# Optimization experiments

Hardware: AMD Instinct MI355X
Metric: run time of the kernel (lower is better)

The kernel has to match this reference:

```python
import jax, jax.numpy as jnp
import numpy as np

NEG_SLOPE = 0.2

def gat_conv(x, edge_index, W, a_src, a_dst, b):
    # PyG GATConv, heads=1, eval mode (dropout off), add_self_loops=True
    N = x.shape[0]
    h = x @ W                                   # [N, C]
    loops = jnp.arange(N, dtype=edge_index.dtype)
    src = jnp.concatenate([edge_index[0], loops])
    dst = jnp.concatenate([edge_index[1], loops])
    s_src = h @ a_src                            # [N]
    s_dst = h @ a_dst                            # [N]
    e = s_src[src] + s_dst[dst]                  # [E+N]
    e = jnp.where(e > 0, e, NEG_SLOPE * e)       # leaky_relu
    # segment softmax over destination neighborhoods
    m = jax.ops.segment_max(e, dst, num_segments=N)
    ex = jnp.exp(e - m[dst])
    denom = jax.ops.segment_sum(ex, dst, num_segments=N)
    alpha = ex / denom[dst]                      # [E+N]
    out = jax.ops.segment_sum(alpha[:, None] * h[src], dst, num_segments=N)
    return out + b

def setup_inputs() -> dict:
    key = jax.random.key(0)
    ks = jax.random.split(key, 10)
    N, F_in, H, C, E = 100000, 256, 128, 40, 1600000
    x = jax.random.normal(ks[0], (N, F_in), dtype=jnp.float32)
    edge_index = jax.random.randint(ks[1], (2, E), 0, N, dtype=jnp.int64)
    s1 = 1.0 / np.sqrt(F_in)
    s2 = 1.0 / np.sqrt(H)
    W1 = jax.random.normal(ks[2], (F_in, H), dtype=jnp.float32) * s1
    a_src1 = jax.random.normal(ks[3], (H,), dtype=jnp.float32) * s2
    a_dst1 = jax.random.normal(ks[4], (H,), dtype=jnp.float32) * s2
    b1 = jnp.zeros((H,), dtype=jnp.float32)
    W2 = jax.random.normal(ks[5], (H, C), dtype=jnp.float32) * s2
    a_src2 = jax.random.normal(ks[6], (C,), dtype=jnp.float32) * 0.1
    a_dst2 = jax.random.normal(ks[7], (C,), dtype=jnp.float32) * 0.1
    b2 = jnp.zeros((C,), dtype=jnp.float32)
    return {"x": x, "edge_index": edge_index, "W1": W1, "a_src1": a_src1,
            "a_dst1": a_dst1, "b1": b1, "W2": W2, "a_src2": a_src2,
            "a_dst2": a_dst2, "b2": b2}

def reference(x, edge_index, W1, a_src1, a_dst1, b1, W2, a_src2, a_dst2, b2):
    h = gat_conv(x, edge_index, W1, a_src1, a_dst1, b1)
    h = jax.nn.relu(h)
    # dropout(p=0.6) is identity in eval mode
    h = gat_conv(h, edge_index, W2, a_src2, a_dst2, b2)
    return jax.nn.log_softmax(h, axis=1)
```

## Files before the change

kernel.cpp:

```cpp
#include <hip/hip_runtime.h>
#include <math.h>

#define NEG_SLOPE 0.2f
#define CAP 64
#define NB 64
#define NBUCKET 1563
#define BCAP 1408
#define CHUNK 8192
#define NBINBLK 196

typedef __attribute__((ext_vector_type(8))) short short8;
typedef __attribute__((ext_vector_type(4))) short short4v;
typedef __attribute__((ext_vector_type(4))) float f32x4;
typedef __attribute__((ext_vector_type(2))) float f32x2;

__device__ inline unsigned short f2bf(float f) {
    union { float f; unsigned u; } x; x.f = f;
    unsigned r = x.u + 0x7FFFu + ((x.u >> 16) & 1u);
    return (unsigned short)(r >> 16);
}

__device__ __forceinline__ void gload_lds16(const void* g, void* l) {
    __builtin_amdgcn_global_load_lds(
        (const __attribute__((address_space(1))) void*)g,
        (__attribute__((address_space(3))) void*)l, 16, 0, 0);
}


__global__ __launch_bounds__(256) void front_kernel(
    const int* __restrict__ ei, int* __restrict__ bcnt,
    unsigned* __restrict__ bbuf, int E,
    const float* __restrict__ W1, const float* __restrict__ W2,
    short* __restrict__ bsw1, short* __restrict__ bsw2)
{
    __shared__ int lc[NBUCKET];
    __shared__ int lsrc[CHUNK];
    __shared__ int ldst[CHUNK];
    const int tid = threadIdx.x;

    if (blockIdx.x < NBINBLK) {
        const int base = blockIdx.x * CHUNK;
        const int n = (E - base < CHUNK) ? (E - base) : CHUNK;

        for (int b = tid; b < NBUCKET; b += 256) lc[b] = 0;
        __syncthreads();

        for (int i = tid; i < n; i += 256) {
            int s = ei[base + i];
            int d = ei[E + base + i];
            lsrc[i] = s;
            ldst[i] = d;
            atomicAdd(&lc[d >> 6], 1);
        }
        __syncthreads();

        for (int b = tid; b < NBUCKET; b += 256) {
            int c = lc[b];
            lc[b] = c ? atomicAdd(&bcnt[b], c) : 0;
        }
        __syncthreads();

        for (int i = tid; i < n; i += 256) {
            int s = lsrc[i];
            int d = ldst[i];
            int b = d >> 6;
            int pos = atomicAdd(&lc[b], 1);
            if (pos < BCAP)
                bbuf[(size_t)b * BCAP + pos] = (unsigned)s | ((unsigned)(d & 63) << 17);
        }
    } else {
        int t = (blockIdx.x - NBINBLK) * 256 + tid;
        if (t < 4096) {
            int lane = t & 63;
            int f = t >> 6;
            int k_step = f & 7;
            int n_tile = f >> 3;
            int n  = n_tile * 16 + (lane & 15);
            int k0 = k_step * 32 + (lane >> 4) * 8;
            short8 v;
            #pragma unroll
            for (int j = 0; j < 8; j++)
                v[j] = (short)f2bf(W1[(size_t)(k0 + j) * 128 + n]);
            ((short8*)bsw1)[t] = v;
        } else if (t < 4096 + 768) {
            int u = t - 4096;
            int lane = u & 63;
            int f = u >> 6;
            int k_step = f & 3;
            int n_tile = f >> 2;
            int n  = n_tile * 16 + (lane & 15);
            int k0 = k_step * 32 + (lane >> 4) * 8;
            short8 v;
            #pragma unroll
            for (int j = 0; j < 8; j++)
                v[j] = (n < 40) ? (short)f2bf(W2[(size_t)(k0 + j) * 40 + n]) : (short)0;
            ((short8*)bsw2)[u] = v;
        }
    }
}

__global__ __launch_bounds__(256) void mid_kernel(
    const int* __restrict__ bcnt, const unsigned* __restrict__ bbuf,
    int* __restrict__ csr, int* __restrict__ sorted, int* __restrict__ clsCnt,
    const float* __restrict__ x, const short* __restrict__ bsw,
    const float* __restrict__ a_src, const float* __restrict__ a_dst,
    unsigned char* __restrict__ h1, float* __restrict__ s_src,
    float* __restrict__ s_dst, int M)
{
    __shared__ __align__(16) char smem[16896];
    const int tid = threadIdx.x;

    if (blockIdx.x < NBUCKET) {
        int* lcnt = (int*)smem;
        int (*lcsr)[CAP] = (int(*)[CAP])(smem + 256);
        int* chist = (int*)(smem + 256 + 16384);
        int* cbase = (int*)(smem + 256 + 16384 + 16);

        const int b = blockIdx.x;
        const int nb = b * NB;

        if (tid < NB) lcnt[tid] = 0;
        if (tid < 4) chist[tid] = 0;
        __syncthreads();

        if (tid < NB && nb + tid < M) {
            int pos = atomicAdd(&lcnt[tid], 1);
            if (pos < CAP) lcsr[tid][pos] = nb + tid;
        }

        int ne = bcnt[b]; if (ne > BCAP) ne = BCAP;
        const unsigned* __restrict__ bp = bbuf + (size_t)b * BCAP;
        for (int j = tid; j < ne; j += 256) {
            unsigned v = bp[j];
            int s  = v & 0x1FFFF;
            int dl = v >> 17;
            int pos = atomicAdd(&lcnt[dl], 1);
            if (pos < CAP) lcsr[dl][pos] = s;
        }
        __syncthreads();

        const int4* __restrict__ srcp = (const int4*)&lcsr[0][0];
        int4* __restrict__ dstp = (int4*)(csr + (size_t)nb * CAP);
        #pragma unroll 4
        for (int j = tid; j < NB * CAP / 4; j += 256) dstp[j] = srcp[j];

        int deg = 0, cls = 0, pos = 0;
        bool isNode = (tid < NB && nb + tid < M);
        if (isNode) {
            deg = lcnt[tid]; if (deg > CAP) deg = CAP;
            cls = (deg - 1) >> 4;
            pos = atomicAdd(&chist[cls], 1);
        }
        __syncthreads();
        if (tid < 4) cbase[tid] = chist[tid] ? atomicAdd(&clsCnt[tid], chist[tid]) : 0;
        __syncthreads();
        if (isNode)
            sorted[(size_t)cls * M + cbase[cls] + pos] = (nb + tid) | (deg << 17);
        return;
    }

    const int wave = tid >> 6, lane = tid & 63;
    short8* lbs = (short8*)smem;
    const int rowBase = (blockIdx.x - NBUCKET) * 64;
    const int arow = rowBase + wave * 16 + (lane & 15);
    const int acol0 = (lane >> 4) * 8;
    const bool rv = (arow < M);
    const float* __restrict__ xr = x + (size_t)arow * 256 + acol0;
    const char* __restrict__ bsb = (const char*)bsw;

    auto stage = [&](int buf, int nt) {
        const char* s = bsb + nt * 8192 + wave * 2048 + lane * 16;
        char* d = smem + buf * 8192 + wave * 2048 + lane * 16;
        gload_lds16(s, d);
        gload_lds16(s + 1024, d + 1024);
    };

    stage(0, 0);

    short8 a[8];
    #pragma unroll
    for (int k = 0; k < 8; k++) {
        float4 p = make_float4(0.f, 0.f, 0.f, 0.f);
        float4 q = p;
        if (rv) {
            p = *(const float4*)(xr + k * 32);
            q = *(const float4*)(xr + k * 32 + 4);
        }
        short8 t;
        t[0] = (short)f2bf(p.x); t[1] = (short)f2bf(p.y);
        t[2] = (short)f2bf(p.z); t[3] = (short)f2bf(p.w);
        t[4] = (short)f2bf(q.x); t[5] = (short)f2bf(q.y);
        t[6] = (short)f2bf(q.z); t[7] = (short)f2bf(q.w);
        a[k] = t;
    }

    const int R0 = rowBase + wave * 16 + (lane >> 4) * 4;
    const int Cb = lane & 15;

    float asv[8], adv[8];
    #pragma unroll
    for (int nt = 0; nt < 8; nt++) {
        asv[nt] = a_src[nt * 16 + Cb];
        adv[nt] = a_dst[nt * 16 + Cb];
    }

    stage(1, 1);

    float ss[4] = {0.f, 0.f, 0.f, 0.f};
    float sd[4] = {0.f, 0.f, 0.f, 0.f};
    f32x4 prev = {0.f, 0.f, 0.f, 0.f};
    int wpk[4][4];

    #pragma unroll
    for (int nt = 0; nt < 8; nt++) {
        if (nt == 7) asm volatile("s_waitcnt vmcnt(0)" ::: "memory");
        else         asm volatile("s_waitcnt vmcnt(2)" ::: "memory");
        __builtin_amdgcn_s_barrier();

        short8 breg[8];
        #pragma unroll
        for (int k = 0; k < 8; k++) breg[k] = lbs[(nt & 1) * 512 + k * 64 + lane];
        asm volatile("s_waitcnt lgkmcnt(0)" ::: "memory");
        __builtin_amdgcn_sched_barrier(0);
        __builtin_amdgcn_s_barrier();

        if (nt < 6) stage(nt & 1, nt + 2);

        f32x4 acc = {0.f, 0.f, 0.f, 0.f};
        #pragma unroll
        for (int k = 0; k < 8; k++)
            acc = __builtin_amdgcn_mfma_f32_16x16x32_bf16(a[k], breg[k], acc, 0, 0, 0);

        float as_ = asv[nt], ad_ = adv[nt];
        #pragma unroll
        for (int r = 0; r < 4; r++) {
            float v = acc[r];
            ss[r] = fmaf(v, as_, ss[r]);
            sd[r] = fmaf(v, ad_, sd[r]);
        }
        if (nt & 1) {
            #pragma unroll
            for (int r = 0; r < 4; r++)
                wpk[nt >> 1][r] = __builtin_amdgcn_cvt_pk_fp8_f32(prev[r], acc[r], 0, false);
        } else {
            prev = acc;
        }
    }

    #pragma unroll
    for (int r = 0; r < 4; r++) {
        int R = R0 + r;
        if (R < M) {
            #pragma unroll
            for (int t = 0; t < 4; t++)
                *(unsigned short*)(h1 + (size_t)R * 128 + t * 32 + 2 * Cb) =
                    (unsigned short)wpk[t][r];
        }
    }
    #pragma unroll
    for (int off = 1; off < 16; off <<= 1) {
        #pragma unroll
        for (int r = 0; r < 4; r++) {
            ss[r] += __shfl_xor(ss[r], off);
            sd[r] += __shfl_xor(sd[r], off);
        }
    }
    if ((lane & 15) == 0) {
        #pragma unroll
        for (int r = 0; r < 4; r++) {
            int R = R0 + r;
            if (R < M) { s_src[R] = ss[r]; s_dst[R] = sd[r]; }
        }
    }
}

__global__ __launch_bounds__(256) void agg1_kernel(
    const unsigned char* __restrict__ h, const int* __restrict__ csr,
    const int* __restrict__ sorted, const int* __restrict__ clsCnt,
    const float* __restrict__ s_src, const float* __restrict__ s_dst,
    const float* __restrict__ bias,
    const short* __restrict__ bsw2,
    const float* __restrict__ a_src2, const float* __restrict__ a_dst2,
    unsigned char* __restrict__ h2, float* __restrict__ ss2,
    float* __restrict__ sd2, int N)
{
    __shared__ short lrow[16][136];
    __shared__ int   lnode[16];
    const int tid = threadIdx.x;
    const int lane = tid & 63;
    const int c = lane & 15;
    const int base = lane & 48;
    const int grp = tid >> 4;
    const int g = blockIdx.x * 16 + grp;

    int c0 = clsCnt[0], c01 = c0 + clsCnt[1], c012 = c01 + clsCnt[2];
    int cls, local;
    if (g < c0)        { cls = 0; local = g; }
    else if (g < c01)  { cls = 1; local = g - c0; }
    else if (g < c012) { cls = 2; local = g - c01; }
    else               { cls = 3; local = g - c012; }

    int ent = sorted[(size_t)cls * N + local];
    int n = ent & 0x1FFFF;
    int deg = ent >> 17;
    const int* __restrict__ edges = csr + (size_t)n * CAP;
    float sdn = s_dst[n];

    int s0 = 0, s1 = 0, s2 = 0, s3 = 0;
    float e0 = -1e30f, e1 = -1e30f, e2 = -1e30f, e3 = -1e30f;
    if (c < deg)      { s0 = edges[c];      e0 = s_src[s0] + sdn; }
    if (c + 16 < deg) { s1 = edges[c + 16]; e1 = s_src[s1] + sdn; }
    if (c + 32 < deg) { s2 = edges[c + 32]; e2 = s_src[s2] + sdn; }
    if (c + 48 < deg) { s3 = edges[c + 48]; e3 = s_src[s3] + sdn; }
    e0 = e0 > 0.f ? e0 : NEG_SLOPE * e0;
    e1 = e1 > 0.f ? e1 : NEG_SLOPE * e1;
    e2 = e2 > 0.f ? e2 : NEG_SLOPE * e2;
    e3 = e3 > 0.f ? e3 : NEG_SLOPE * e3;
    float m = fmaxf(fmaxf(e0, e1), fmaxf(e2, e3));
    #pragma unroll
    for (int off = 1; off < 16; off <<= 1) m = fmaxf(m, __shfl_xor(m, off));
    float w0 = (c < deg)      ? __expf(e0 - m) : 0.f;
    float w1 = (c + 16 < deg) ? __expf(e1 - m) : 0.f;
    float w2 = (c + 32 < deg) ? __expf(e2 - m) : 0.f;
    float w3 = (c + 48 < deg) ? __expf(e3 - m) : 0.f;
    float denom = (w0 + w1) + (w2 + w3);
    #pragma unroll
    for (int off = 1; off < 16; off <<= 1) denom += __shfl_xor(denom, off);
    float inv = 1.0f / denom;

    const uint2* __restrict__ hp = (const uint2*)h;
    f32x2 acc0 = {0.f, 0.f}, acc1 = {0.f, 0.f}, acc2 = {0.f, 0.f}, acc3 = {0.f, 0.f};

#define AGG1_BLK(K, SK, WK)                                                  \
    if (16 * K < deg) {                                                      \
        _Pragma("unroll")                                                    \
        for (int jj = 0; jj < 16; jj++) {                                    \
            int   sv = __shfl(SK, base + jj);                                \
            float wv = __shfl(WK, base + jj);                                \
            if (16 * K + jj < deg) {                                         \
                uint2 u = hp[(size_t)sv * 16 + c];                           \
                f32x2 p;                                                     \
                p = __builtin_amdgcn_cvt_pk_f32_fp8(u.x, false); acc0 += p * wv; \
                p = __builtin_amdgcn_cvt_pk_f32_fp8(u.x, true);  acc1 += p * wv; \
                p = __builtin_amdgcn_cvt_pk_f32_fp8(u.y, false); acc2 += p * wv; \
                p = __builtin_amdgcn_cvt_pk_f32_fp8(u.y, true);  acc3 += p * wv; \
            }                                                                \
        }                                                                    \
    }
    AGG1_BLK(0, s0, w0)
    AGG1_BLK(1, s1, w1)
    AGG1_BLK(2, s2, w2)
    AGG1_BLK(3, s3, w3)
#undef AGG1_BLK

    int cA = 32 * (c >> 2) + 4 * (c & 3);
    float4 bA = *(const float4*)&bias[cA];
    float4 bB = *(const float4*)&bias[cA + 16];
    float r0 = fmaxf(fmaf(acc0.x, inv, bA.x), 0.f);
    float r1 = fmaxf(fmaf(acc1.x, inv, bA.y), 0.f);
    float r2 = fmaxf(fmaf(acc2.x, inv, bA.z), 0.f);
    float r3 = fmaxf(fmaf(acc3.x, inv, bA.w), 0.f);
    float q0 = fmaxf(fmaf(acc0.y, inv, bB.x), 0.f);
    float q1 = fmaxf(fmaf(acc1.y, inv, bB.y), 0.f);
    float q2 = fmaxf(fmaf(acc2.y, inv, bB.z), 0.f);
    float q3 = fmaxf(fmaf(acc3.y, inv, bB.w), 0.f);
    short4v oA = { (short)f2bf(r0), (short)f2bf(r1), (short)f2bf(r2), (short)f2bf(r3) };
    short4v oB = { (short)f2bf(q0), (short)f2bf(q1), (short)f2bf(q2), (short)f2bf(q3) };
    *(short4v*)&lrow[grp][cA] = oA;
    *(short4v*)&lrow[grp][cA + 16] = oB;
    if (c == 0) lnode[grp] = n;
    __syncthreads();

    if (tid >= 64) return;

    const short8* __restrict__ bs = (const short8*)bsw2;
    short8 a[4];
    #pragma unroll
    for (int k = 0; k < 4; k++)
        a[k] = *(const short8*)&lrow[lane & 15][(lane >> 4) * 8 + k * 32];

    float accs[3][4];
    float ssv[4] = {0.f, 0.f, 0.f, 0.f};
    float sdv[4] = {0.f, 0.f, 0.f, 0.f};

    #pragma unroll
    for (int nt = 0; nt < 3; nt++) {
        f32x4 acc = {0.f, 0.f, 0.f, 0.f};
        #pragma unroll
        for (int k = 0; k < 4; k++) {
            short8 b = bs[(nt * 4 + k) * 64 + lane];
            acc = __builtin_amdgcn_mfma_f32_16x16x32_bf16(a[k], b, acc, 0, 0, 0);
        }
        int C = nt * 16 + c;
        bool valid = (C < 40);
        float as_ = valid ? a_src2[C] : 0.f;
        float ad_ = valid ? a_dst2[C] : 0.f;
        #pragma unroll
        for (int r = 0; r < 4; r++) {
            float v = acc[r];
            accs[nt][r] = v;
            ssv[r] = fmaf(v, as_, ssv[r]);
            sdv[r] = fmaf(v, ad_, sdv[r]);
        }
    }
    #pragma unroll
    for (int r = 0; r < 4; r++) {
        int node = lnode[(lane >> 4) * 4 + r];
        int wA = __builtin_amdgcn_cvt_pk_fp8_f32(accs[0][r], accs[1][r], 0, false);
        int wB = __builtin_amdgcn_cvt_pk_fp8_f32(accs[2][r], 0.f, 0, false);
        *(unsigned short*)(h2 + (size_t)node * 64 + 2 * c) = (unsigned short)wA;
        *(unsigned short*)(h2 + (size_t)node * 64 + 32 + 2 * c) = (unsigned short)wB;
    }
    #pragma unroll
    for (int off = 1; off < 16; off <<= 1) {
        #pragma unroll
        for (int r = 0; r < 4; r++) {
            ssv[r] += __shfl_xor(ssv[r], off);
            sdv[r] += __shfl_xor(sdv[r], off);
        }
    }
    if (c == 0) {
        #pragma unroll
        for (int r = 0; r < 4; r++) {
            int node = lnode[(lane >> 4) * 4 + r];
            ss2[node] = ssv[r];
            sd2[node] = sdv[r];
        }
    }
}

__global__ __launch_bounds__(256) void agg2_kernel(
    const unsigned char* __restrict__ h, const int* __restrict__ csr,
    const int* __restrict__ sorted, const int* __restrict__ clsCnt,
    const float* __restrict__ s_src, const float* __restrict__ s_dst,
    const float* __restrict__ bias, float* __restrict__ out, int N)
{
    const int lane = threadIdx.x & 63;
    const int c = lane & 15;
    const int base = lane & 48;
    const int g = blockIdx.x * 16 + (threadIdx.x >> 4);

    int c0 = clsCnt[0], c01 = c0 + clsCnt[1], c012 = c01 + clsCnt[2];
    int cls, local;
    if (g < c0)        { cls = 0; local = g; }
    else if (g < c01)  { cls = 1; local = g - c0; }
    else if (g < c012) { cls = 2; local = g - c01; }
    else               { cls = 3; local = g - c012; }

    int ent = sorted[(size_t)cls * N + local];
    int n = ent & 0x1FFFF;
    int deg = ent >> 17;
    const int* __restrict__ edges = csr + (size_t)n * CAP;
    float sdn = s_dst[n];

    int s0 = 0, s1 = 0, s2 = 0, s3 = 0;
    float e0 = -1e30f, e1 = -1e30f, e2 = -1e30f, e3 = -1e30f;
    if (c < deg)      { s0 = edges[c];      e0 = s_src[s0] + sdn; }
    if (c + 16 < deg) { s1 = edges[c + 16]; e1 = s_src[s1] + sdn; }
    if (c + 32 < deg) { s2 = edges[c + 32]; e2 = s_src[s2] + sdn; }
    if (c + 48 < deg) { s3 = edges[c + 48]; e3 = s_src[s3] + sdn; }
    e0 = e0 > 0.f ? e0 : NEG_SLOPE * e0;
    e1 = e1 > 0.f ? e1 : NEG_SLOPE * e1;
    e2 = e2 > 0.f ? e2 : NEG_SLOPE * e2;
    e3 = e3 > 0.f ? e3 : NEG_SLOPE * e3;
    float m = fmaxf(fmaxf(e0, e1), fmaxf(e2, e3));
    #pragma unroll
    for (int off = 1; off < 16; off <<= 1) m = fmaxf(m, __shfl_xor(m, off));
    float w0 = (c < deg)      ? __expf(e0 - m) : 0.f;
    float w1 = (c + 16 < deg) ? __expf(e1 - m) : 0.f;
    float w2 = (c + 32 < deg) ? __expf(e2 - m) : 0.f;
    float w3 = (c + 48 < deg) ? __expf(e3 - m) : 0.f;
    float denom = (w0 + w1) + (w2 + w3);
    #pragma unroll
    for (int off = 1; off < 16; off <<= 1) denom += __shfl_xor(denom, off);
    float inv = 1.0f / denom;

    const unsigned* __restrict__ hp = (const unsigned*)h;
    f32x2 acc0 = {0.f, 0.f}, acc1 = {0.f, 0.f};

#define AGG2_BLK(K, SK, WK)                                                  \
    if (16 * K < deg) {                                                      \
        _Pragma("unroll")                                                    \
        for (int jj = 0; jj < 16; jj++) {                                    \
            int   sv = __shfl(SK, base + jj);                                \
            float wv = __shfl(WK, base + jj);                                \
            if (16 * K + jj < deg) {                                         \
                unsigned u = hp[(size_t)sv * 16 + c];                        \
                f32x2 p;                                                     \
                p = __builtin_amdgcn_cvt_pk_f32_fp8(u, false); acc0 += p * wv; \
                p = __builtin_amdgcn_cvt_pk_f32_fp8(u, true);  acc1 += p * wv; \
            }                                                                \
        }                                                                    \
    }
    AGG2_BLK(0, s0, w0)
    AGG2_BLK(1, s1, w1)
    AGG2_BLK(2, s2, w2)
    AGG2_BLK(3, s3, w3)
#undef AGG2_BLK

    float v0 = -1e30f, v1 = -1e30f, v2 = -1e30f, v3 = -1e30f;
    bool has01 = (c < 8), has0 = (c < 12);
    if (has01) {
        v0 = fmaf(acc0.x, inv, bias[2*c]);
        v1 = fmaf(acc0.y, inv, bias[2*c + 16]);
        v2 = fmaf(acc1.x, inv, bias[2*c + 1]);
        v3 = fmaf(acc1.y, inv, bias[2*c + 17]);
    } else if (has0) {
        v0 = fmaf(acc0.x, inv, bias[2*c + 16]);
        v2 = fmaf(acc1.x, inv, bias[2*c + 17]);
    }

    float mx = fmaxf(fmaxf(v0, v1), fmaxf(v2, v3));
    #pragma unroll
    for (int off = 1; off < 16; off <<= 1) mx = fmaxf(mx, __shfl_xor(mx, off));
    float sum = 0.f;
    if (has01) sum = __expf(v0 - mx) + __expf(v1 - mx) + __expf(v2 - mx) + __expf(v3 - mx);
    else if (has0) sum = __expf(v0 - mx) + __expf(v2 - mx);
    #pragma unroll
    for (int off = 1; off < 16; off <<= 1) sum += __shfl_xor(sum, off);
    float lg = mx + __logf(sum);

    if (has01) {
        *(float2*)&out[(size_t)n * 40 + 2*c]      = make_float2(v0 - lg, v2 - lg);
        *(float2*)&out[(size_t)n * 40 + 2*c + 16] = make_float2(v1 - lg, v3 - lg);
    } else if (has0) {
        *(float2*)&out[(size_t)n * 40 + 2*c + 16] = make_float2(v0 - lg, v2 - lg);
    }
}

extern "C" void kernel_launch(void* const* d_in, const int* in_sizes, int n_in,
                              void* d_out, int out_size, void* d_ws, size_t ws_size,
                              hipStream_t stream)
{
    const float* x      = (const float*)d_in[0];
    const int*   ei     = (const int*)d_in[1];
    const float* W1     = (const float*)d_in[2];
    const float* a_src1 = (const float*)d_in[3];
    const float* a_dst1 = (const float*)d_in[4];
    const float* b1     = (const float*)d_in[5];
    const float* W2     = (const float*)d_in[6];
    const float* a_src2 = (const float*)d_in[7];
    const float* a_dst2 = (const float*)d_in[8];
    const float* b2     = (const float*)d_in[9];
    float* out = (float*)d_out;

    const int N = 100000;
    const int E = 1600000;

    char* ws = (char*)d_ws;
    size_t off = 0;
    auto alloc = [&](size_t bytes) -> void* {
        void* p = ws + off;
        off += (bytes + 255) & ~(size_t)255;
        return p;
    };
    unsigned char*  h1b  = (unsigned char*)alloc((size_t)N * 128);
    unsigned char*  h2b  = (unsigned char*)alloc((size_t)N * 64);
    int*   csr    = (int*)alloc((size_t)NBUCKET * NB * CAP * 4);
    int*   sorted = (int*)alloc((size_t)4 * N * 4);
    float* ss1  = (float*)alloc((size_t)N * 4);
    float* sd1  = (float*)alloc((size_t)N * 4);
    float* ss2  = (float*)alloc((size_t)N * 4);
    float* sd2  = (float*)alloc((size_t)N * 4);
    short* bsw1 = (short*)alloc((size_t)4096 * 8 * 2);
    short* bsw2 = (short*)alloc((size_t)768 * 8 * 2);
    int*   bcnt = (int*)alloc((size_t)(NBUCKET + 4) * 4);
    int*   clsCnt = bcnt + NBUCKET;
    unsigned* bbuf = (unsigned*)alloc((size_t)NBUCKET * BCAP * 4);

    hipMemsetAsync(bcnt, 0, (size_t)(NBUCKET + 4) * 4, stream);

    front_kernel<<<dim3(NBINBLK + 19), dim3(256), 0, stream>>>(
        ei, bcnt, bbuf, E, W1, W2, bsw1, bsw2);

    mid_kernel<<<dim3(NBUCKET + (N + 63) / 64), dim3(256), 0, stream>>>(
        bcnt, bbuf, csr, sorted, clsCnt,
        x, bsw1, a_src1, a_dst1, h1b, ss1, sd1, N);

    agg1_kernel<<<dim3(N / 16), dim3(256), 0, stream>>>(
        h1b, csr, sorted, clsCnt, ss1, sd1, b1,
        bsw2, a_src2, a_dst2, h2b, ss2, sd2, N);

    agg2_kernel<<<dim3(N / 16), dim3(256), 0, stream>>>(
        h2b, csr, sorted, clsCnt, ss2, sd2, b2, out, N);
}
```

Baseline: 339.2 us.

## Batch neighbor gathers, split edge binning finer, and add occupancy launch bounds

The agg1 and agg2 kernels now issue all 16 neighbor row loads of a block before converting and accumulating them, and drop the per-edge degree check. This raises memory-level parallelism on the gathers and relies on padded slots holding a valid source index with zero weight. The mid kernel hoists its x loads ahead of the bf16 conversion. The front binning kernel uses smaller 2048-edge chunks over more blocks and rereads edge_index instead of staging it in LDS, which cuts LDS use and raises occupancy at the cost of a second global read. Launch-bounds hints ask for 2 to 4 blocks per CU, which can force register spills.

```diff
diff --git a/kernel.cpp b/kernel.cpp
--- a/kernel.cpp
+++ b/kernel.cpp
@@ -6,8 +6,8 @@
 #define NB 64
 #define NBUCKET 1563
 #define BCAP 1408
-#define CHUNK 8192
-#define NBINBLK 196
+#define BINCHUNK 2048
+#define NBIN2 782
 
 typedef __attribute__((ext_vector_type(8))) short short8;
 typedef __attribute__((ext_vector_type(4))) short short4v;
@@ -34,42 +34,32 @@
     short* __restrict__ bsw1, short* __restrict__ bsw2)
 {
     __shared__ int lc[NBUCKET];
-    __shared__ int lsrc[CHUNK];
-    __shared__ int ldst[CHUNK];
     const int tid = threadIdx.x;
 
-    if (blockIdx.x < NBINBLK) {
-        const int base = blockIdx.x * CHUNK;
-        const int n = (E - base < CHUNK) ? (E - base) : CHUNK;
+    if (blockIdx.x < NBIN2) {
+        const int base = blockIdx.x * BINCHUNK;
+        int n = E - base; if (n > BINCHUNK) n = BINCHUNK;
 
         for (int b = tid; b < NBUCKET; b += 256) lc[b] = 0;
         __syncthreads();
-
+        for (int i = tid; i < n; i += 256)
+            atomicAdd(&lc[ei[E + base + i] >> 6], 1);
+        __syncthreads();
+        for (int b = tid; b < NBUCKET; b += 256) {
+            int c = lc[b];
+            lc[b] = c ? atomicAdd(&bcnt[b], c) : 0;
+        }
+        __syncthreads();
         for (int i = tid; i < n; i += 256) {
             int s = ei[base + i];
             int d = ei[E + base + i];
-            lsrc[i] = s;
-            ldst[i] = d;
-            atomicAdd(&lc[d >> 6], 1);
-        }
-        __syncthreads();
-
-        for (int b = tid; b < NBUCKET; b += 256) {
-            int c = lc[b];
-            lc[b] = c ? atomicAdd(&bcnt[b], c) : 0;
-        }
-        __syncthreads();
-
-        for (int i = tid; i < n; i += 256) {
-            int s = lsrc[i];
-            int d = ldst[i];
             int b = d >> 6;
             int pos = atomicAdd(&lc[b], 1);
             if (pos < BCAP)
                 bbuf[(size_t)b * BCAP + pos] = (unsigned)s | ((unsigned)(d & 63) << 17);
         }
     } else {
-        int t = (blockIdx.x - NBINBLK) * 256 + tid;
+        int t = (blockIdx.x - NBIN2) * 256 + tid;
         if (t < 4096) {
             int lane = t & 63;
             int f = t >> 6;
@@ -99,7 +89,7 @@
     }
 }
 
-__global__ __launch_bounds__(256) void mid_kernel(
+__global__ __launch_bounds__(256, 2) void mid_kernel(
     const int* __restrict__ bcnt, const unsigned* __restrict__ bbuf,
     int* __restrict__ csr, int* __restrict__ sorted, int* __restrict__ clsCnt,
     const float* __restrict__ x, const short* __restrict__ bsw,
@@ -177,20 +167,24 @@
 
     stage(0, 0);
 
+    float4 px[8], qx[8];
+    #pragma unroll
+    for (int k = 0; k < 8; k++) {
+        px[k] = make_float4(0.f, 0.f, 0.f, 0.f);
+        qx[k] = px[k];
+        if (rv) {
+            px[k] = *(const float4*)(xr + k * 32);
+            qx[k] = *(const float4*)(xr + k * 32 + 4);
+        }
+    }
     short8 a[8];
     #pragma unroll
     for (int k = 0; k < 8; k++) {
-        float4 p = make_float4(0.f, 0.f, 0.f, 0.f);
-        float4 q = p;
-        if (rv) {
-            p = *(const float4*)(xr + k * 32);
-            q = *(const float4*)(xr + k * 32 + 4);
-        }
         short8 t;
-        t[0] = (short)f2bf(p.x); t[1] = (short)f2bf(p.y);
-        t[2] = (short)f2bf(p.z); t[3] = (short)f2bf(p.w);
-        t[4] = (short)f2bf(q.x); t[5] = (short)f2bf(q.y);
-        t[6] = (short)f2bf(q.z); t[7] = (short)f2bf(q.w);
+        t[0] = (short)f2bf(px[k].x); t[1] = (short)f2bf(px[k].y);
+        t[2] = (short)f2bf(px[k].z); t[3] = (short)f2bf(px[k].w);
+        t[4] = (short)f2bf(qx[k].x); t[5] = (short)f2bf(qx[k].y);
+        t[6] = (short)f2bf(qx[k].z); t[7] = (short)f2bf(qx[k].w);
         a[k] = t;
     }
 
@@ -274,7 +268,7 @@
     }
 }
 
-__global__ __launch_bounds__(256) void agg1_kernel(
+__global__ __launch_bounds__(256, 4) void agg1_kernel(
     const unsigned char* __restrict__ h, const int* __restrict__ csr,
     const int* __restrict__ sorted, const int* __restrict__ clsCnt,
     const float* __restrict__ s_src, const float* __restrict__ s_dst,
@@ -333,18 +327,20 @@
 
 #define AGG1_BLK(K, SK, WK)                                                  \
     if (16 * K < deg) {                                                      \
+        uint2 u[16];                                                         \
         _Pragma("unroll")                                                    \
         for (int jj = 0; jj < 16; jj++) {                                    \
-            int   sv = __shfl(SK, base + jj);                                \
+            int sv = __shfl(SK, base + jj);                                  \
+            u[jj] = hp[(size_t)sv * 16 + c];                                 \
+        }                                                                    \
+        _Pragma("unroll")                                                    \
+        for (int jj = 0; jj < 16; jj++) {                                    \
             float wv = __shfl(WK, base + jj);                                \
-            if (16 * K + jj < deg) {                                         \
-                uint2 u = hp[(size_t)sv * 16 + c];                           \
-                f32x2 p;                                                     \
-                p = __builtin_amdgcn_cvt_pk_f32_fp8(u.x, false); acc0 += p * wv; \
-                p = __builtin_amdgcn_cvt_pk_f32_fp8(u.x, true);  acc1 += p * wv; \
-                p = __builtin_amdgcn_cvt_pk_f32_fp8(u.y, false); acc2 += p * wv; \
-                p = __builtin_amdgcn_cvt_pk_f32_fp8(u.y, true);  acc3 += p * wv; \
-            }                                                                \
+            f32x2 p;                                                         \
+            p = __builtin_amdgcn_cvt_pk_f32_fp8(u[jj].x, false); acc0 += p * wv; \
+            p = __builtin_amdgcn_cvt_pk_f32_fp8(u[jj].x, true);  acc1 += p * wv; \
+            p = __builtin_amdgcn_cvt_pk_f32_fp8(u[jj].y, false); acc2 += p * wv; \
+            p = __builtin_amdgcn_cvt_pk_f32_fp8(u[jj].y, true);  acc3 += p * wv; \
         }                                                                    \
     }
     AGG1_BLK(0, s0, w0)
@@ -429,7 +425,7 @@
     }
 }
 
-__global__ __launch_bounds__(256) void agg2_kernel(
+__global__ __launch_bounds__(256, 4) void agg2_kernel(
     const unsigned char* __restrict__ h, const int* __restrict__ csr,
     const int* __restrict__ sorted, const int* __restrict__ clsCnt,
     const float* __restrict__ s_src, const float* __restrict__ s_dst,
@@ -480,16 +476,18 @@
 
 #define AGG2_BLK(K, SK, WK)                                                  \
     if (16 * K < deg) {                                                      \
+        unsigned u[16];                                                      \
         _Pragma("unroll")                                                    \
         for (int jj = 0; jj < 16; jj++) {                                    \
-            int   sv = __shfl(SK, base + jj);                                \
+            int sv = __shfl(SK, base + jj);                                  \
+            u[jj] = hp[(size_t)sv * 16 + c];                                 \
+        }                                                                    \
+        _Pragma("unroll")                                                    \
+        for (int jj = 0; jj < 16; jj++) {                                    \
             float wv = __shfl(WK, base + jj);                                \
-            if (16 * K + jj < deg) {                                         \
-                unsigned u = hp[(size_t)sv * 16 + c];                        \
-                f32x2 p;                                                     \
-                p = __builtin_amdgcn_cvt_pk_f32_fp8(u, false); acc0 += p * wv; \
-                p = __builtin_amdgcn_cvt_pk_f32_fp8(u, true);  acc1 += p * wv; \
-            }                                                                \
+            f32x2 p;                                                         \
+            p = __builtin_amdgcn_cvt_pk_f32_fp8(u[jj], false); acc0 += p * wv; \
+            p = __builtin_amdgcn_cvt_pk_f32_fp8(u[jj], true);  acc1 += p * wv; \
         }                                                                    \
     }
     AGG2_BLK(0, s0, w0)
@@ -570,7 +568,7 @@
 
     hipMemsetAsync(bcnt, 0, (size_t)(NBUCKET + 4) * 4, stream);
 
-    front_kernel<<<dim3(NBINBLK + 19), dim3(256), 0, stream>>>(
+    front_kernel<<<dim3(NBIN2 + 19), dim3(256), 0, stream>>>(
         ei, bcnt, bbuf, E, W1, W2, bsw1, bsw2);
 
     mid_kernel<<<dim3(NBUCKET + (N + 63) / 64), dim3(256), 0, stream>>>(
```

After: 331.5 us. -2.3%, faster.
